# Optimization experiments

Measured on AMD Instinct MI355X. Metric: run time of the kernel, lower is better.

## Reference

```python
import jax, jax.numpy as jnp
import numpy as np

D_MODEL = 1024
NUM_HEADS = 16
D_K = D_MODEL // NUM_HEADS
B, S = 2, 2048


def setup_inputs() -> dict:
    key = jax.random.key(0)
    ks = jax.random.split(key, 11)
    sc = 1.0 / np.sqrt(D_MODEL)
    inp = {
        "query": jax.random.normal(ks[0], (B, S, D_MODEL), jnp.float32),
        "key": jax.random.normal(ks[1], (B, S, D_MODEL), jnp.float32),
        "value": jax.random.normal(ks[2], (B, S, D_MODEL), jnp.float32),
        "Wq": jax.random.normal(ks[3], (D_MODEL, D_MODEL), jnp.float32) * sc,
        "bq": jax.random.normal(ks[4], (D_MODEL,), jnp.float32) * sc,
        "Wk": jax.random.normal(ks[5], (D_MODEL, D_MODEL), jnp.float32) * sc,
        "bk": jax.random.normal(ks[6], (D_MODEL,), jnp.float32) * sc,
        "Wv": jax.random.normal(ks[7], (D_MODEL, D_MODEL), jnp.float32) * sc,
        "bv": jax.random.normal(ks[8], (D_MODEL,), jnp.float32) * sc,
        "Wo": jax.random.normal(ks[9], (D_MODEL, D_MODEL), jnp.float32) * sc,
        "bo": jax.random.normal(ks[10], (D_MODEL,), jnp.float32) * sc,
    }
    return inp


def reference(query, key, value, Wq, bq, Wk, bk, Wv, bv, Wo, bo):
    b = query.shape[0]
    # Linear projections (torch Linear: x @ W.T + b), W is [out, in]
    Q = query @ Wq.T + bq
    K = key @ Wk.T + bk
    V = value @ Wv.T + bv
    # [B, S, D] -> [B, H, S, d_k]
    Q = Q.reshape(b, -1, NUM_HEADS, D_K).transpose(0, 2, 1, 3)
    K = K.reshape(b, -1, NUM_HEADS, D_K).transpose(0, 2, 1, 3)
    V = V.reshape(b, -1, NUM_HEADS, D_K).transpose(0, 2, 1, 3)
    # Scaled dot-product attention (mask=None, dropout inactive in eval)
    scores = jnp.einsum("bhqd,bhkd->bhqk", Q, K) / jnp.sqrt(jnp.float32(D_K))
    attn = jax.nn.softmax(scores, axis=-1)
    out = jnp.einsum("bhqk,bhkd->bhqd", attn, V)
    # [B, H, S, d_k] -> [B, S, D]
    out = out.transpose(0, 2, 1, 3).reshape(b, -1, D_MODEL)
    return out @ Wo.T + bo
```

## Files before the change

### kernel.cpp

```cpp
#include <hip/hip_runtime.h>

typedef __bf16 bf16x8 __attribute__((ext_vector_type(8)));
typedef __bf16 bf16x4 __attribute__((ext_vector_type(4)));
typedef float f32x4 __attribute__((ext_vector_type(4)));

#define D_MODEL 1024
#define NUM_HEADS 16
#define DK 64
#define BATCH 2
#define SEQ 2048
#define M_ROWS (BATCH*SEQ)

#define QSCALE 0.18033688011112042f

#if defined(__has_builtin)
#if __has_builtin(__builtin_amdgcn_exp2f)
#define EXP2(x) __builtin_amdgcn_exp2f(x)
#endif
#endif
#ifndef EXP2
#define EXP2(x) exp2f(x)
#endif

#define GLOAD_LDS16(gp, lp) __builtin_amdgcn_global_load_lds( \
    (__attribute__((address_space(1))) void*)(gp), \
    (__attribute__((address_space(3))) void*)(lp), 16, 0, 0)

#define ACT ((size_t)M_ROWS * D_MODEL)
#define WSZ ((size_t)D_MODEL * D_MODEL)

__global__ __launch_bounds__(256) void cvt_all(
    const float* __restrict__ q, const float* __restrict__ k,
    const float* __restrict__ v, const float* __restrict__ wq,
    const float* __restrict__ wk, const float* __restrict__ wv,
    const float* __restrict__ wo, __bf16* __restrict__ dst)
{
  size_t e = ((size_t)blockIdx.x * 256 + threadIdx.x) * 8;
  const float* s;
  size_t off;
  if (e < 3 * ACT) {
    int t = (int)(e >> 22);
    s = t == 0 ? q : (t == 1 ? k : v);
    off = e & (ACT - 1);
  } else {
    size_t e2 = e - 3 * ACT;
    int t = (int)(e2 >> 20);
    s = t == 0 ? wq : (t == 1 ? wk : (t == 2 ? wv : wo));
    off = e2 & (WSZ - 1);
  }
  float4 a = *(const float4*)(s + off);
  float4 b = *(const float4*)(s + off + 4);
  bf16x8 o;
  o[0] = (__bf16)a.x; o[1] = (__bf16)a.y; o[2] = (__bf16)a.z; o[3] = (__bf16)a.w;
  o[4] = (__bf16)b.x; o[5] = (__bf16)b.y; o[6] = (__bf16)b.z; o[7] = (__bf16)b.w;
  *(bf16x8*)(dst + e) = o;
}

template <typename OutT, int MI>
__device__ __forceinline__ void gemm_body(
    const __bf16* __restrict__ A, const __bf16* __restrict__ W,
    const float* __restrict__ bias, OutT* __restrict__ C,
    int M, int N, int K, int m0, int n0, float scale)
{
  __shared__ __align__(16) __bf16 sA[2][MI*32*64];
  __shared__ __align__(16) __bf16 sB[2][64*64];
  const int tid  = threadIdx.x;
  const int wave = tid >> 6;
  const int lane = tid & 63;
  const int l16  = lane & 15;
  const int quad = lane >> 4;
  const int wm = (wave >> 1) * (MI * 16);
  const int wn = (wave & 1) * 32;

  f32x4 acc[MI][2] = {};

  const int gsw = (((tid & 7) ^ ((tid >> 3) & 7))) * 8;
  long aoff[MI], boff[2];
#pragma unroll
  for (int i = 0; i < MI; i++) {
    int row = (i * 256 + tid) >> 3;
    aoff[i] = (long)(m0 + row) * K + gsw;
  }
#pragma unroll
  for (int i = 0; i < 2; i++) {
    int row = (i * 256 + tid) >> 3;
    boff[i] = (long)(n0 + row) * K + gsw;
  }
  const int rsw = l16 & 7;

  const int NT = K / 64;

#pragma unroll
  for (int i = 0; i < MI; i++)
    GLOAD_LDS16(A + aoff[i], (char*)sA[0] + i * 4096 + tid * 16);
#pragma unroll
  for (int i = 0; i < 2; i++)
    GLOAD_LDS16(W + boff[i], (char*)sB[0] + i * 4096 + tid * 16);
  __syncthreads();

  for (int t = 0; t < NT; t++) {
    const __bf16* sAc = sA[t & 1];
    const __bf16* sBc = sB[t & 1];
    if (t + 1 < NT) {
      int k1 = (t + 1) * 64;
      char* sAn = (char*)sA[(t + 1) & 1];
      char* sBn = (char*)sB[(t + 1) & 1];
#pragma unroll
      for (int i = 0; i < MI; i++)
        GLOAD_LDS16(A + aoff[i] + k1, sAn + i * 4096 + tid * 16);
#pragma unroll
      for (int i = 0; i < 2; i++)
        GLOAD_LDS16(W + boff[i] + k1, sBn + i * 4096 + tid * 16);
    }
#pragma unroll
    for (int ks = 0; ks < 2; ks++) {
      bf16x8 af[MI], bf[2];
#pragma unroll
      for (int i = 0; i < MI; i++)
        af[i] = *(const bf16x8*)&sAc[(wm + i * 16 + l16) * 64 + ((ks * 4 + quad) ^ rsw) * 8];
#pragma unroll
      for (int j = 0; j < 2; j++)
        bf[j] = *(const bf16x8*)&sBc[(wn + j * 16 + l16) * 64 + ((ks * 4 + quad) ^ rsw) * 8];
#pragma unroll
      for (int i = 0; i < MI; i++)
#pragma unroll
        for (int j = 0; j < 2; j++)
          acc[i][j] = __builtin_amdgcn_mfma_f32_16x16x32_bf16(af[i], bf[j], acc[i][j], 0, 0, 0);
    }
    if (t + 1 < NT) __syncthreads();
  }

#pragma unroll
  for (int j = 0; j < 2; j++) {
    int col = n0 + wn + j * 16 + l16;
    float bv = bias[col];
#pragma unroll
    for (int i = 0; i < MI; i++) {
      long row0 = m0 + wm + i * 16 + quad * 4;
#pragma unroll
      for (int r = 0; r < 4; r++)
        C[(row0 + r) * N + col] = (OutT)((acc[i][j][r] + bv) * scale);
    }
  }
}

__global__ __launch_bounds__(256) void gemm_qkv(
    const __bf16* __restrict__ Abase, const __bf16* __restrict__ Wbase,
    const float* __restrict__ b0, const float* __restrict__ b1,
    const float* __restrict__ b2, __bf16* __restrict__ Cbase)
{
  int lid = blockIdx.x + (blockIdx.y << 4) + (blockIdx.z << 9);
  int swz = (lid & 7) * 192 + (lid >> 3);
  int x = swz & 15, y = (swz >> 4) & 31, z = swz >> 9;
  const __bf16* A = Abase + (size_t)z * M_ROWS * D_MODEL;
  const __bf16* W = Wbase + (size_t)z * D_MODEL * D_MODEL;
  const float* bias = z == 0 ? b0 : (z == 1 ? b1 : b2);
  float scale = z == 0 ? QSCALE : 1.0f;
  __bf16* C = Cbase + (size_t)z * M_ROWS * D_MODEL;
  gemm_body<__bf16, 4>(A, W, bias, C, M_ROWS, D_MODEL, D_MODEL,
                       y * 128, x * 64, scale);
}

__global__ __launch_bounds__(256) void gemm_out(
    const __bf16* __restrict__ A, const __bf16* __restrict__ W,
    const float* __restrict__ bias, float* __restrict__ C)
{
  int lid = blockIdx.x + (blockIdx.y << 4);
  int swz = (lid & 7) * 128 + (lid >> 3);
  int x = swz & 15, y = swz >> 4;
  gemm_body<float, 2>(A, W, bias, C, M_ROWS, D_MODEL, D_MODEL,
                      y * 64, x * 64, 1.0f);
}

__global__ __launch_bounds__(512) void attn_kernel(
    const __bf16* __restrict__ Q, const __bf16* __restrict__ K,
    const __bf16* __restrict__ V, __bf16* __restrict__ O)
{
  constexpr int SV_LD = 136;

  __shared__ __align__(16) __bf16 sK[128 * 64];
  __shared__ __align__(16) __bf16 sVt[DK * SV_LD];
  __shared__ float lsbuf[8][16];

  const int tid  = threadIdx.x;
  const int wave = tid >> 6;
  const int g    = wave & 3;
  const int kh   = wave >> 2;
  const int lane = tid & 63;
  const int l16  = lane & 15;
  const int quad = lane >> 4;

  const int bh = blockIdx.y;
  const int b  = bh >> 4, h = bh & (NUM_HEADS - 1);
  const int q0 = blockIdx.x * 64;
  const long base = (long)b * SEQ * D_MODEL + h * DK;

  const __bf16* qrow = Q + base + (long)(q0 + g * 16 + l16) * D_MODEL + quad * 8;
  const bf16x8 aq0 = *(const bf16x8*)(qrow);
  const bf16x8 aq1 = *(const bf16x8*)(qrow + 32);

  const int gsw = (((tid & 7) ^ ((tid >> 3) & 7))) * 8;
  const __bf16* kp[2];
#pragma unroll
  for (int i = 0; i < 2; i++)
    kp[i] = K + base + (long)((i * 512 + tid) >> 3) * D_MODEL + gsw;
  const int rsw = l16 & 7;

  const __bf16* vp0 = V + base + (long)(2 * lane) * D_MODEL + wave * 8;
  const int k5 = (2 * lane) & 31;
  const int pos5 = ((k5 & 12) << 1) | ((k5 & 16) >> 2) | (k5 & 3);
  const int vcol = (lane >> 4) * 16 + (pos5 >> 1);

  uint4 kr0 = *(const uint4*)(kp[0]);
  uint4 kr1 = *(const uint4*)(kp[1]);
  uint4 vr0 = *(const uint4*)(vp0);
  uint4 vr1 = *(const uint4*)(vp0 + D_MODEL);

  f32x4 lacc = {};
  f32x4 o[4] = {};

  for (int t = 0; t < SEQ / 128; t++) {
    __syncthreads();
    *(uint4*)((char*)sK + tid * 16) = kr0;
    *(uint4*)((char*)sK + 8192 + tid * 16) = kr1;
    {
      const ushort* e0 = (const ushort*)&vr0;
      const ushort* e1 = (const ushort*)&vr1;
      uint* dst = (uint*)sVt;
#pragma unroll
      for (int j = 0; j < 8; j++)
        dst[(wave * 8 + j) * (SV_LD / 2) + vcol] = (uint)e0[j] | ((uint)e1[j] << 16);
    }
    if (t + 1 < SEQ / 128) {
      long adv = (long)(t + 1) * 128 * D_MODEL;
      kr0 = *(const uint4*)(kp[0] + adv);
      kr1 = *(const uint4*)(kp[1] + adv);
      vr0 = *(const uint4*)(vp0 + adv);
      vr1 = *(const uint4*)(vp0 + adv + D_MODEL);
    }
    __syncthreads();

#pragma unroll
    for (int kl = 0; kl < 2; kl++) {
      const int kt = kh * 2 + kl;
      bf16x8 af;
#pragma unroll
      for (int hh = 0; hh < 2; hh++) {
        int nt = kt * 2 + hh;
        bf16x8 b0 = *(const bf16x8*)&sK[(nt * 16 + l16) * 64 + (quad ^ rsw) * 8];
        bf16x8 b1 = *(const bf16x8*)&sK[(nt * 16 + l16) * 64 + ((4 + quad) ^ rsw) * 8];
        f32x4 z = {};
        __builtin_amdgcn_s_setprio(1);
        z = __builtin_amdgcn_mfma_f32_16x16x32_bf16(b0, aq0, z, 0, 0, 0);
        z = __builtin_amdgcn_mfma_f32_16x16x32_bf16(b1, aq1, z, 0, 0, 0);
        __builtin_amdgcn_s_setprio(0);
        f32x4 p;
#pragma unroll
        for (int r = 0; r < 4; r++) p[r] = EXP2(z[r]);
        lacc += p;
#pragma unroll
        for (int r = 0; r < 4; r++) af[hh * 4 + r] = (__bf16)p[r];
      }
      __builtin_amdgcn_s_setprio(1);
#pragma unroll
      for (int dt = 0; dt < 4; dt++) {
        bf16x8 bv = *(const bf16x8*)&sVt[(dt * 16 + l16) * SV_LD + kt * 32 + quad * 8];
        o[dt] = __builtin_amdgcn_mfma_f32_16x16x32_bf16(af, bv, o[dt], 0, 0, 0);
      }
      __builtin_amdgcn_s_setprio(0);
    }
  }

  float ls = lacc[0] + lacc[1] + lacc[2] + lacc[3];
  ls += __shfl_xor(ls, 16, 64);
  ls += __shfl_xor(ls, 32, 64);

  __syncthreads();
  if (quad == 0) lsbuf[wave][l16] = ls;
  f32x4* scr = (f32x4*)sK;
  if (kh == 1) {
#pragma unroll
    for (int dt = 0; dt < 4; dt++)
      scr[dt * 256 + g * 64 + lane] = o[dt];
  }
  __syncthreads();
  if (kh == 0) {
    float lst = lsbuf[g][l16] + lsbuf[4 + g][l16];
    float rls[4];
#pragma unroll
    for (int r = 0; r < 4; r++)
      rls[r] = 1.0f / __shfl(lst, quad * 4 + r, 64);
#pragma unroll
    for (int dt = 0; dt < 4; dt++) {
      f32x4 oo = o[dt] + scr[dt * 256 + g * 64 + lane];
#pragma unroll
      for (int r = 0; r < 4; r++) {
        int s = q0 + g * 16 + quad * 4 + r;
        int d = dt * 16 + l16;
        O[base + (long)s * D_MODEL + d] = (__bf16)(oo[r] * rls[r]);
      }
    }
  }
}

extern "C" void kernel_launch(void* const* d_in, const int* in_sizes, int n_in,
                              void* d_out, int out_size, void* d_ws, size_t ws_size,
                              hipStream_t stream) {
  const float* q  = (const float*)d_in[0];
  const float* k  = (const float*)d_in[1];
  const float* v  = (const float*)d_in[2];
  const float* Wq = (const float*)d_in[3];
  const float* bq = (const float*)d_in[4];
  const float* Wk = (const float*)d_in[5];
  const float* bk = (const float*)d_in[6];
  const float* Wv = (const float*)d_in[7];
  const float* bv = (const float*)d_in[8];
  const float* Wo = (const float*)d_in[9];
  const float* bo = (const float*)d_in[10];
  float* out = (float*)d_out;

  __bf16* qc  = (__bf16*)d_ws;
  __bf16* Wqc = qc + 3 * ACT;
  __bf16* wsQ = Wqc + 4 * WSZ;
  __bf16* wsAo = qc;

  dim3 blk(256);
  cvt_all<<<dim3((3 * ACT + 4 * WSZ) / 2048), blk, 0, stream>>>(
      q, k, v, Wq, Wk, Wv, Wo, qc);

  gemm_qkv<<<dim3(D_MODEL / 64, M_ROWS / 128, 3), blk, 0, stream>>>(
      qc, Wqc, bq, bk, bv, wsQ);

  attn_kernel<<<dim3(SEQ / 64, BATCH * NUM_HEADS), dim3(512), 0, stream>>>(
      wsQ, wsQ + ACT, wsQ + 2 * ACT, wsAo);

  gemm_out<<<dim3(16, 64), blk, 0, stream>>>(
      wsAo, Wqc + 3 * WSZ, bo, out);
}
```

Baseline: 230.5 us.

## Triple-buffer GEMM LDS loads with explicit vmcnt waits; enlarge output GEMM tile

```diff
diff --git a/kernel.cpp b/kernel.cpp
--- a/kernel.cpp
+++ b/kernel.cpp
@@ -62,8 +62,8 @@
     const float* __restrict__ bias, OutT* __restrict__ C,
     int M, int N, int K, int m0, int n0, float scale)
 {
-  __shared__ __align__(16) __bf16 sA[2][MI*32*64];
-  __shared__ __align__(16) __bf16 sB[2][64*64];
+  __shared__ __align__(16) __bf16 sA[3][MI*32*64];
+  __shared__ __align__(16) __bf16 sB[3][64*64];
   const int tid  = threadIdx.x;
   const int wave = tid >> 6;
   const int lane = tid & 63;
@@ -89,22 +89,28 @@
   const int rsw = l16 & 7;
 
   const int NT = K / 64;
-
-#pragma unroll
-  for (int i = 0; i < MI; i++)
-    GLOAD_LDS16(A + aoff[i], (char*)sA[0] + i * 4096 + tid * 16);
-#pragma unroll
-  for (int i = 0; i < 2; i++)
-    GLOAD_LDS16(W + boff[i], (char*)sB[0] + i * 4096 + tid * 16);
-  __syncthreads();
+  constexpr int LPS = MI + 2;
+
+  {
+#pragma unroll
+    for (int i = 0; i < MI; i++)
+      GLOAD_LDS16(A + aoff[i], (char*)sA[0] + i * 4096 + tid * 16);
+#pragma unroll
+    for (int i = 0; i < 2; i++)
+      GLOAD_LDS16(W + boff[i], (char*)sB[0] + i * 4096 + tid * 16);
+#pragma unroll
+    for (int i = 0; i < MI; i++)
+      GLOAD_LDS16(A + aoff[i] + 64, (char*)sA[1] + i * 4096 + tid * 16);
+#pragma unroll
+    for (int i = 0; i < 2; i++)
+      GLOAD_LDS16(W + boff[i] + 64, (char*)sB[1] + i * 4096 + tid * 16);
+  }
 
   for (int t = 0; t < NT; t++) {
-    const __bf16* sAc = sA[t & 1];
-    const __bf16* sBc = sB[t & 1];
-    if (t + 1 < NT) {
-      int k1 = (t + 1) * 64;
-      char* sAn = (char*)sA[(t + 1) & 1];
-      char* sBn = (char*)sB[(t + 1) & 1];
+    if (t + 2 < NT) {
+      int k1 = (t + 2) * 64;
+      char* sAn = (char*)sA[(t + 2) % 3];
+      char* sBn = (char*)sB[(t + 2) % 3];
 #pragma unroll
       for (int i = 0; i < MI; i++)
         GLOAD_LDS16(A + aoff[i] + k1, sAn + i * 4096 + tid * 16);
@@ -112,6 +118,17 @@
       for (int i = 0; i < 2; i++)
         GLOAD_LDS16(W + boff[i] + k1, sBn + i * 4096 + tid * 16);
     }
+    if (t + 2 < NT)
+      asm volatile("s_waitcnt vmcnt(%0)" :: "n"(2 * LPS) : "memory");
+    else if (t + 1 < NT)
+      asm volatile("s_waitcnt vmcnt(%0)" :: "n"(LPS) : "memory");
+    else
+      asm volatile("s_waitcnt vmcnt(0)" ::: "memory");
+    __builtin_amdgcn_s_barrier();
+    __builtin_amdgcn_sched_barrier(0);
+
+    const __bf16* sAc = sA[t % 3];
+    const __bf16* sBc = sB[t % 3];
 #pragma unroll
     for (int ks = 0; ks < 2; ks++) {
       bf16x8 af[MI], bf[2];
@@ -127,7 +144,10 @@
         for (int j = 0; j < 2; j++)
           acc[i][j] = __builtin_amdgcn_mfma_f32_16x16x32_bf16(af[i], bf[j], acc[i][j], 0, 0, 0);
     }
-    if (t + 1 < NT) __syncthreads();
+    if (t + 1 < NT) {
+      __builtin_amdgcn_sched_barrier(0);
+      __builtin_amdgcn_s_barrier();
+    }
   }
 
 #pragma unroll
@@ -166,10 +186,10 @@
     const float* __restrict__ bias, float* __restrict__ C)
 {
   int lid = blockIdx.x + (blockIdx.y << 4);
-  int swz = (lid & 7) * 128 + (lid >> 3);
+  int swz = (lid & 7) * 64 + (lid >> 3);
   int x = swz & 15, y = swz >> 4;
-  gemm_body<float, 2>(A, W, bias, C, M_ROWS, D_MODEL, D_MODEL,
-                      y * 64, x * 64, 1.0f);
+  gemm_body<float, 4>(A, W, bias, C, M_ROWS, D_MODEL, D_MODEL,
+                      y * 128, x * 64, 1.0f);
 }
 
 __global__ __launch_bounds__(512) void attn_kernel(
@@ -334,6 +354,6 @@
   attn_kernel<<<dim3(SEQ / 64, BATCH * NUM_HEADS), dim3(512), 0, stream>>>(
       wsQ, wsQ + ACT, wsQ + 2 * ACT, wsAo);
 
-  gemm_out<<<dim3(16, 64), blk, 0, stream>>>(
+  gemm_out<<<dim3(16, 32), blk, 0, stream>>>(
       wsAo, Wqc + 3 * WSZ, bo, out);
 }
```

Result: no change. 229.0 us (-0.6%).

## Fuse fp32-to-bf16 conversion into GEMM loads via register-staged tiles

Applied to the files above, without the earlier changes.

```diff
diff --git a/kernel.cpp b/kernel.cpp
--- a/kernel.cpp
+++ b/kernel.cpp
@@ -22,48 +22,17 @@
 #define EXP2(x) exp2f(x)
 #endif
 
-#define GLOAD_LDS16(gp, lp) __builtin_amdgcn_global_load_lds( \
-    (__attribute__((address_space(1))) void*)(gp), \
-    (__attribute__((address_space(3))) void*)(lp), 16, 0, 0)
-
 #define ACT ((size_t)M_ROWS * D_MODEL)
 #define WSZ ((size_t)D_MODEL * D_MODEL)
 
-__global__ __launch_bounds__(256) void cvt_all(
-    const float* __restrict__ q, const float* __restrict__ k,
-    const float* __restrict__ v, const float* __restrict__ wq,
-    const float* __restrict__ wk, const float* __restrict__ wv,
-    const float* __restrict__ wo, __bf16* __restrict__ dst)
-{
-  size_t e = ((size_t)blockIdx.x * 256 + threadIdx.x) * 8;
-  const float* s;
-  size_t off;
-  if (e < 3 * ACT) {
-    int t = (int)(e >> 22);
-    s = t == 0 ? q : (t == 1 ? k : v);
-    off = e & (ACT - 1);
-  } else {
-    size_t e2 = e - 3 * ACT;
-    int t = (int)(e2 >> 20);
-    s = t == 0 ? wq : (t == 1 ? wk : (t == 2 ? wv : wo));
-    off = e2 & (WSZ - 1);
-  }
-  float4 a = *(const float4*)(s + off);
-  float4 b = *(const float4*)(s + off + 4);
-  bf16x8 o;
-  o[0] = (__bf16)a.x; o[1] = (__bf16)a.y; o[2] = (__bf16)a.z; o[3] = (__bf16)a.w;
-  o[4] = (__bf16)b.x; o[5] = (__bf16)b.y; o[6] = (__bf16)b.z; o[7] = (__bf16)b.w;
-  *(bf16x8*)(dst + e) = o;
-}
-
-template <typename OutT, int MI>
-__device__ __forceinline__ void gemm_body(
-    const __bf16* __restrict__ A, const __bf16* __restrict__ W,
+template <typename OutT, int MI, bool CA, bool CB>
+__device__ __forceinline__ void gemm_body_rs(
+    const void* __restrict__ Av, const void* __restrict__ Wv,
     const float* __restrict__ bias, OutT* __restrict__ C,
     int M, int N, int K, int m0, int n0, float scale)
 {
-  __shared__ __align__(16) __bf16 sA[2][MI*32*64];
-  __shared__ __align__(16) __bf16 sB[2][64*64];
+  __shared__ __align__(16) __bf16 sA[MI*32*64];
+  __shared__ __align__(16) __bf16 sB[64*64];
   const int tid  = threadIdx.x;
   const int wave = tid >> 6;
   const int lane = tid & 63;
@@ -72,6 +41,11 @@
   const int wm = (wave >> 1) * (MI * 16);
   const int wn = (wave & 1) * 32;
 
+  const float*  A32 = (const float*)Av;
+  const __bf16* A16 = (const __bf16*)Av;
+  const float*  W32 = (const float*)Wv;
+  const __bf16* W16 = (const __bf16*)Wv;
+
   f32x4 acc[MI][2] = {};
 
   const int gsw = (((tid & 7) ^ ((tid >> 3) & 7))) * 8;
@@ -90,44 +64,84 @@
 
   const int NT = K / 64;
 
-#pragma unroll
-  for (int i = 0; i < MI; i++)
-    GLOAD_LDS16(A + aoff[i], (char*)sA[0] + i * 4096 + tid * 16);
-#pragma unroll
-  for (int i = 0; i < 2; i++)
-    GLOAD_LDS16(W + boff[i], (char*)sB[0] + i * 4096 + tid * 16);
-  __syncthreads();
+  float4 a0[MI], a1[MI]; uint4 aU[MI];
+  float4 b0[2],  b1[2];  uint4 bU[2];
+
+  auto loadT = [&](int kk) {
+#pragma unroll
+    for (int i = 0; i < MI; i++) {
+      if constexpr (CA) {
+        a0[i] = *(const float4*)(A32 + aoff[i] + kk);
+        a1[i] = *(const float4*)(A32 + aoff[i] + kk + 4);
+      } else {
+        aU[i] = *(const uint4*)(A16 + aoff[i] + kk);
+      }
+    }
+#pragma unroll
+    for (int i = 0; i < 2; i++) {
+      if constexpr (CB) {
+        b0[i] = *(const float4*)(W32 + boff[i] + kk);
+        b1[i] = *(const float4*)(W32 + boff[i] + kk + 4);
+      } else {
+        bU[i] = *(const uint4*)(W16 + boff[i] + kk);
+      }
+    }
+  };
+
+  auto writeS = [&]() {
+#pragma unroll
+    for (int i = 0; i < MI; i++) {
+      if constexpr (CA) {
+        bf16x8 w;
+#pragma unroll
+        for (int e = 0; e < 4; e++) {
+          w[e]     = (__bf16)((&a0[i].x)[e]);
+          w[4 + e] = (__bf16)((&a1[i].x)[e]);
+        }
+        *(bf16x8*)((char*)sA + i * 4096 + tid * 16) = w;
+      } else {
+        *(uint4*)((char*)sA + i * 4096 + tid * 16) = aU[i];
+      }
+    }
+#pragma unroll
+    for (int i = 0; i < 2; i++) {
+      if constexpr (CB) {
+        bf16x8 w;
+#pragma unroll
+        for (int e = 0; e < 4; e++) {
+          w[e]     = (__bf16)((&b0[i].x)[e]);
+          w[4 + e] = (__bf16)((&b1[i].x)[e]);
+        }
+        *(bf16x8*)((char*)sB + i * 4096 + tid * 16) = w;
+      } else {
+        *(uint4*)((char*)sB + i * 4096 + tid * 16) = bU[i];
+      }
+    }
+  };
+
+  loadT(0);
 
   for (int t = 0; t < NT; t++) {
-    const __bf16* sAc = sA[t & 1];
-    const __bf16* sBc = sB[t & 1];
-    if (t + 1 < NT) {
-      int k1 = (t + 1) * 64;
-      char* sAn = (char*)sA[(t + 1) & 1];
-      char* sBn = (char*)sB[(t + 1) & 1];
-#pragma unroll
-      for (int i = 0; i < MI; i++)
-        GLOAD_LDS16(A + aoff[i] + k1, sAn + i * 4096 + tid * 16);
-#pragma unroll
-      for (int i = 0; i < 2; i++)
-        GLOAD_LDS16(W + boff[i] + k1, sBn + i * 4096 + tid * 16);
-    }
+    __syncthreads();
+    writeS();
+    if (t + 1 < NT) loadT((t + 1) * 64);
+    __syncthreads();
+
 #pragma unroll
     for (int ks = 0; ks < 2; ks++) {
       bf16x8 af[MI], bf[2];
 #pragma unroll
       for (int i = 0; i < MI; i++)
-        af[i] = *(const bf16x8*)&sAc[(wm + i * 16 + l16) * 64 + ((ks * 4 + quad) ^ rsw) * 8];
+        af[i] = *(const bf16x8*)&sA[(wm + i * 16 + l16) * 64 + ((ks * 4 + quad) ^ rsw) * 8];
 #pragma unroll
       for (int j = 0; j < 2; j++)
-        bf[j] = *(const bf16x8*)&sBc[(wn + j * 16 + l16) * 64 + ((ks * 4 + quad) ^ rsw) * 8];
+        bf[j] = *(const bf16x8*)&sB[(wn + j * 16 + l16) * 64 + ((ks * 4 + quad) ^ rsw) * 8];
 #pragma unroll
       for (int i = 0; i < MI; i++)
 #pragma unroll
         for (int j = 0; j < 2; j++)
           acc[i][j] = __builtin_amdgcn_mfma_f32_16x16x32_bf16(af[i], bf[j], acc[i][j], 0, 0, 0);
     }
-    if (t + 1 < NT) __syncthreads();
   }
 
 #pragma unroll
@@ -145,31 +159,33 @@
 }
 
 __global__ __launch_bounds__(256) void gemm_qkv(
-    const __bf16* __restrict__ Abase, const __bf16* __restrict__ Wbase,
+    const float* __restrict__ x_q, const float* __restrict__ x_k,
+    const float* __restrict__ x_v, const float* __restrict__ Wq,
+    const float* __restrict__ Wk, const float* __restrict__ Wv,
     const float* __restrict__ b0, const float* __restrict__ b1,
     const float* __restrict__ b2, __bf16* __restrict__ Cbase)
 {
   int lid = blockIdx.x + (blockIdx.y << 4) + (blockIdx.z << 9);
   int swz = (lid & 7) * 192 + (lid >> 3);
   int x = swz & 15, y = (swz >> 4) & 31, z = swz >> 9;
-  const __bf16* A = Abase + (size_t)z * M_ROWS * D_MODEL;
-  const __bf16* W = Wbase + (size_t)z * D_MODEL * D_MODEL;
+  const float* A = z == 0 ? x_q : (z == 1 ? x_k : x_v);
+  const float* W = z == 0 ? Wq : (z == 1 ? Wk : Wv);
   const float* bias = z == 0 ? b0 : (z == 1 ? b1 : b2);
   float scale = z == 0 ? QSCALE : 1.0f;
   __bf16* C = Cbase + (size_t)z * M_ROWS * D_MODEL;
-  gemm_body<__bf16, 4>(A, W, bias, C, M_ROWS, D_MODEL, D_MODEL,
-                       y * 128, x * 64, scale);
+  gemm_body_rs<__bf16, 4, true, true>(A, W, bias, C, M_ROWS, D_MODEL, D_MODEL,
+                                      y * 128, x * 64, scale);
 }
 
 __global__ __launch_bounds__(256) void gemm_out(
-    const __bf16* __restrict__ A, const __bf16* __restrict__ W,
+    const __bf16* __restrict__ A, const float* __restrict__ W,
     const float* __restrict__ bias, float* __restrict__ C)
 {
   int lid = blockIdx.x + (blockIdx.y << 4);
-  int swz = (lid & 7) * 128 + (lid >> 3);
+  int swz = (lid & 7) * 64 + (lid >> 3);
   int x = swz & 15, y = swz >> 4;
-  gemm_body<float, 2>(A, W, bias, C, M_ROWS, D_MODEL, D_MODEL,
-                      y * 64, x * 64, 1.0f);
+  gemm_body_rs<float, 4, false, true>(A, W, bias, C, M_ROWS, D_MODEL, D_MODEL,
+                                      y * 128, x * 64, 1.0f);
 }
 
 __global__ __launch_bounds__(512) void attn_kernel(
@@ -319,21 +335,17 @@
   const float* bo = (const float*)d_in[10];
   float* out = (float*)d_out;
 
-  __bf16* qc  = (__bf16*)d_ws;
-  __bf16* Wqc = qc + 3 * ACT;
-  __bf16* wsQ = Wqc + 4 * WSZ;
-  __bf16* wsAo = qc;
+  __bf16* wsQ  = (__bf16*)d_ws;
+  __bf16* wsAo = wsQ + 3 * ACT;
 
   dim3 blk(256);
-  cvt_all<<<dim3((3 * ACT + 4 * WSZ) / 2048), blk, 0, stream>>>(
-      q, k, v, Wq, Wk, Wv, Wo, qc);
 
   gemm_qkv<<<dim3(D_MODEL / 64, M_ROWS / 128, 3), blk, 0, stream>>>(
-      qc, Wqc, bq, bk, bv, wsQ);
+      q, k, v, Wq, Wk, Wv, bq, bk, bv, wsQ);
 
   attn_kernel<<<dim3(SEQ / 64, BATCH * NUM_HEADS), dim3(512), 0, stream>>>(
       wsQ, wsQ + ACT, wsQ + 2 * ACT, wsAo);
 
-  gemm_out<<<dim3(16, 64), blk, 0, stream>>>(
-      wsAo, Wqc + 3 * WSZ, bo, out);
-}
+  gemm_out<<<dim3(16, 32), blk, 0, stream>>>(
+      wsAo, Wo, bo, out);
+}
```

Result: slower. 277.5 us (+20.4%).
